# Kernel optimization log

Measured on AMD Instinct MI355X. Metric: run time of the kernel, lower is better.

Reference implementation:

```python
import jax, jax.numpy as jnp
from jax import lax
import numpy as np

INPUT_SIZE, HIDDEN, NUM_LAYERS, NUM_CLASSES = 128, 256, 2, 100
B, T = 256, 512


def _lstm_layer(x, W_ih, W_hh, b_ih, b_hh):
    # x: [B, T, in]; W_ih: [4H, in]; W_hh: [4H, H]; gate order i,f,g,o (PyTorch)
    Bsz = x.shape[0]
    H = W_hh.shape[1]
    x_proj = jnp.einsum('bti,gi->btg', x, W_ih) + b_ih + b_hh  # [B, T, 4H]
    h0 = jnp.zeros((Bsz, H), x.dtype)
    c0 = jnp.zeros((Bsz, H), x.dtype)

    def step(carry, xt):
        h, c = carry
        gates = xt + h @ W_hh.T  # [B, 4H]
        i, f, g, o = jnp.split(gates, 4, axis=-1)
        i = jax.nn.sigmoid(i)
        f = jax.nn.sigmoid(f)
        g = jnp.tanh(g)
        o = jax.nn.sigmoid(o)
        c = f * c + i * g
        h = o * jnp.tanh(c)
        return (h, c), h

    _, hs = lax.scan(step, (h0, c0), jnp.swapaxes(x_proj, 0, 1))  # hs: [T, B, H]
    return jnp.swapaxes(hs, 0, 1)  # [B, T, H]


def setup_inputs() -> dict:
    key = jax.random.key(0)
    ks = jax.random.split(key, 12)
    s_in = 1.0 / np.sqrt(HIDDEN)
    inp = {
        'x': jax.random.normal(ks[0], (B, T, INPUT_SIZE), jnp.float32),
        'W_ih0': jax.random.uniform(ks[1], (4 * HIDDEN, INPUT_SIZE), jnp.float32, -s_in, s_in),
        'W_hh0': jax.random.uniform(ks[2], (4 * HIDDEN, HIDDEN), jnp.float32, -s_in, s_in),
        'b_ih0': jax.random.uniform(ks[3], (4 * HIDDEN,), jnp.float32, -s_in, s_in),
        'b_hh0': jax.random.uniform(ks[4], (4 * HIDDEN,), jnp.float32, -s_in, s_in),
        'W_ih1': jax.random.uniform(ks[5], (4 * HIDDEN, HIDDEN), jnp.float32, -s_in, s_in),
        'W_hh1': jax.random.uniform(ks[6], (4 * HIDDEN, HIDDEN), jnp.float32, -s_in, s_in),
        'b_ih1': jax.random.uniform(ks[7], (4 * HIDDEN,), jnp.float32, -s_in, s_in),
        'b_hh1': jax.random.uniform(ks[8], (4 * HIDDEN,), jnp.float32, -s_in, s_in),
        'fc_w': jax.random.uniform(ks[9], (NUM_CLASSES, HIDDEN), jnp.float32, -s_in, s_in),
        'fc_b': jax.random.uniform(ks[10], (NUM_CLASSES,), jnp.float32, -s_in, s_in),
    }
    return inp


def reference(x, W_ih0, W_hh0, b_ih0, b_hh0, W_ih1, W_hh1, b_ih1, b_hh1, fc_w, fc_b):
    h = _lstm_layer(x, W_ih0, W_hh0, b_ih0, b_hh0)
    h = _lstm_layer(h, W_ih1, W_hh1, b_ih1, b_hh1)
    return h[:, -1, :] @ fc_w.T + fc_b  # [B, num_classes]
```

## Files before the change

### kernel.cpp

```cpp
#include <hip/hip_runtime.h>
#include <math.h>

namespace {

constexpr int kB  = 256;
constexpr int kT  = 512;
constexpr int kIn = 128;
constexpr int kH  = 256;
constexpr int kG  = 1024;
constexpr int kNC = 100;
constexpr int kCT = 64;
constexpr int kNCh = kT / kCT;

typedef __bf16 bf16x8 __attribute__((ext_vector_type(8)));
typedef float f32x4 __attribute__((ext_vector_type(4)));
typedef int i32x4 __attribute__((ext_vector_type(4)));
typedef unsigned short u16;
static_assert(sizeof(bf16x8) == 16, "bf16x8 must be 4 VGPRs");

__device__ __forceinline__ float sigm(float x) {
  return __builtin_amdgcn_rcpf(1.0f + __expf(-x));
}
__device__ __forceinline__ float tanh_f(float x) {
  const float e = __expf(-2.0f * x);
  return (1.0f - e) * __builtin_amdgcn_rcpf(1.0f + e);
}
__device__ __forceinline__ u16 f2bf(float f) {
  return __builtin_bit_cast(u16, (__bf16)f);
}
__device__ __forceinline__ float bf2f(u16 v) {
  return __builtin_bit_cast(float, ((unsigned)v) << 16);
}

__device__ __forceinline__ void glds16(const void* g, void* l) {
  __builtin_amdgcn_global_load_lds(
      (const __attribute__((address_space(1))) void*)g,
      (__attribute__((address_space(3))) void*)l, 16, 0, 0);
}
__device__ __forceinline__ void glds16_llc(const void* g, void* l) {
  __builtin_amdgcn_global_load_lds(
      (const __attribute__((address_space(1))) void*)g,
      (__attribute__((address_space(3))) void*)l, 16, 0, 17);
}
__device__ __forceinline__ void st_bf16_llc(u16* p, u16 v) {
  asm volatile("global_store_short %0, %1, off sc0 sc1"
               :: "v"((unsigned long long)(uintptr_t)p), "v"(v) : "memory");
}
__device__ __forceinline__ void st_i32_llc(int* p, int v) {
  asm volatile("global_store_dword %0, %1, off sc0 sc1"
               :: "v"((unsigned long long)(uintptr_t)p), "v"(v) : "memory");
}
__device__ __forceinline__ int poll16_min(const int* p) {
  i32x4 a, b, c, d;
  asm volatile(
      "global_load_dwordx4 %0, %4, off sc0 sc1\n\t"
      "global_load_dwordx4 %1, %5, off sc0 sc1\n\t"
      "global_load_dwordx4 %2, %6, off sc0 sc1\n\t"
      "global_load_dwordx4 %3, %7, off sc0 sc1\n\t"
      "s_waitcnt vmcnt(0)"
      : "=v"(a), "=v"(b), "=v"(c), "=v"(d)
      : "v"((unsigned long long)(uintptr_t)p),
        "v"((unsigned long long)(uintptr_t)(p + 4)),
        "v"((unsigned long long)(uintptr_t)(p + 8)),
        "v"((unsigned long long)(uintptr_t)(p + 12))
      : "memory");
  int m = a.x;
  m = min(m, a.y); m = min(m, a.z); m = min(m, a.w);
  m = min(m, b.x); m = min(m, b.y); m = min(m, b.z); m = min(m, b.w);
  m = min(m, c.x); m = min(m, c.y); m = min(m, c.z); m = min(m, c.w);
  m = min(m, d.x); m = min(m, d.y); m = min(m, d.z); m = min(m, d.w);
  return m;
}

__global__ __launch_bounds__(256) void pack_whh_frag(
    const float* __restrict__ whh, u16* __restrict__ wpk) {
  const int idx = blockIdx.x * 256 + threadIdx.x;
  const int e  = idx & 7;
  const int l  = (idx >> 3) & 63;
  const int kb = (idx >> 9) & 7;
  const int g  = (idx >> 12) & 3;
  const int wv = idx >> 14;
  const int n = (g << 8) | (wv << 4) | (l & 15);
  const int k = (kb << 5) | (((l >> 4) & 3) << 3) | e;
  wpk[idx] = f2bf(whh[n * kH + k]);
}

template <int K>
__global__ __launch_bounds__(256) void pack_wih_frag(
    const float* __restrict__ w, u16* __restrict__ wp) {
  constexpr int kbBits = (K == 128) ? 2 : 3;
  const int idx = blockIdx.x * 256 + threadIdx.x;
  const int e  = idx & 7;
  const int l  = (idx >> 3) & 63;
  const int kb = (idx >> 9) & ((K / 32) - 1);
  const int n16 = idx >> (9 + kbBits);
  const int n = (n16 << 4) | (l & 15);
  const int k = (kb << 5) | (((l >> 4) & 3) << 3) | e;
  wp[idx] = f2bf(w[n * K + k]);
}

__global__ __launch_bounds__(256) void conv_x(
    const float* __restrict__ x, u16* __restrict__ xbf) {
  const int f4 = blockIdx.x * 256 + threadIdx.x;
  const int rowid = f4 >> 5;
  const int c4 = f4 & 31;
  const int b = rowid >> 9, t = rowid & 511;
  const float4 v = reinterpret_cast<const float4*>(x)[f4];
  ushort4 o;
  o.x = f2bf(v.x); o.y = f2bf(v.y); o.z = f2bf(v.z); o.w = f2bf(v.w);
  reinterpret_cast<ushort4*>(xbf)[(t * 256 + b) * 32 + c4] = o;
}

template <int K>
__global__ __launch_bounds__(256, 4) void gemm_mfma(
    const u16* __restrict__ A, const u16* __restrict__ Bp,
    const float* __restrict__ b1, const float* __restrict__ b2,
    u16* __restrict__ P2) {
  constexpr int NKB = K / 32;
  const int g = blockIdx.x, mt = blockIdx.y;
  const int tt = mt >> 2, bq = mt & 3;
  const int tid = threadIdx.x, w = tid >> 6, l = tid & 63;

  __shared__ __align__(16) unsigned char smem[40960];
  u16* albuf = (u16*)smem;
  u16* bbuf  = (u16*)(smem + 8192);
  u16* sout  = (u16*)smem;

  const u16* Ab = A + ((size_t)(tt * 256 + bq * 64 + w * 16 + (l & 15))) * K +
                  ((l >> 4) & 3) * 8;
  const u16* Bb = Bp + ((size_t)((g * 16 + w * 4) * NKB) * 64 + l) * 8;

  float bb[4];
#pragma unroll
  for (int j = 0; j < 4; ++j) {
    const int n = g * 256 + (w * 4 + j) * 16 + (l & 15);
    bb[j] = b1[n] + b2[n];
  }

  f32x4 acc[4][4];
#pragma unroll
  for (int mf = 0; mf < 4; ++mf)
#pragma unroll
    for (int nf = 0; nf < 4; ++nf) acc[mf][nf] = f32x4{0.f, 0.f, 0.f, 0.f};

#define STAGE(kb, buf)                                                     \
  {                                                                        \
    glds16(Ab + (kb) * 32, albuf + ((buf) * 4 + w) * 512);                 \
    _Pragma("unroll") for (int j = 0; j < 4; ++j)                          \
        glds16(Bb + ((size_t)(j * NKB + (kb)) * 64) * 8,                   \
               bbuf + ((buf) * 16 + w * 4 + j) * 512);                     \
  }

  STAGE(0, 0);
#pragma unroll
  for (int kb = 0; kb < NKB; ++kb) {
    __syncthreads();
    if (kb + 1 < NKB) STAGE(kb + 1, (kb + 1) & 1);
    const int buf = kb & 1;
    bf16x8 af[4], bf[4];
#pragma unroll
    for (int mf = 0; mf < 4; ++mf)
      af[mf] = *reinterpret_cast<const bf16x8*>(albuf + (buf * 4 + mf) * 512 + l * 8);
#pragma unroll
    for (int nf = 0; nf < 4; ++nf)
      bf[nf] = *reinterpret_cast<const bf16x8*>(bbuf + (buf * 16 + w * 4 + nf) * 512 + l * 8);
#pragma unroll
    for (int mf = 0; mf < 4; ++mf)
#pragma unroll
      for (int nf = 0; nf < 4; ++nf)
        acc[mf][nf] = __builtin_amdgcn_mfma_f32_16x16x32_bf16(
            af[mf], bf[nf], acc[mf][nf], 0, 0, 0);
  }
#undef STAGE

  __syncthreads();
#pragma unroll
  for (int mf = 0; mf < 4; ++mf)
#pragma unroll
    for (int nf = 0; nf < 4; ++nf) {
      ushort4 p;
      p.x = f2bf(acc[mf][nf][0] + bb[nf]);
      p.y = f2bf(acc[mf][nf][1] + bb[nf]);
      p.z = f2bf(acc[mf][nf][2] + bb[nf]);
      p.w = f2bf(acc[mf][nf][3] + bb[nf]);
      *reinterpret_cast<ushort4*>(
          sout + (mf * 16 + w * 4 + nf) * 256 + (l & 15) * 16 + ((l >> 4) & 3) * 4) = p;
    }
  __syncthreads();
#pragma unroll
  for (int i = 0; i < 8; ++i) {
    const int chunk = i * 8 + (tid >> 5);
    const int mf = chunk >> 4, wc = chunk & 15;
    const size_t dst =
        ((((size_t)(bq * 4 + mf) * 64 + tt) * 16 + wc) * 4 + g) * 256 +
        (tid & 31) * 8;
    *reinterpret_cast<uint4*>(P2 + dst) =
        *reinterpret_cast<const uint4*>(sout + (mf * 16 + wc) * 256 + (tid & 31) * 8);
  }
}

__global__ __launch_bounds__(256, 1) void lstm_rec_dual(
    const u16* __restrict__ P2_0, const u16* __restrict__ wpk_0,
    float* __restrict__ cs_0, u16* __restrict__ Ho_0, float* __restrict__ hl_0,
    u16* __restrict__ hx_0, int* __restrict__ tg_0, int first_0,
    const u16* __restrict__ P2_1, const u16* __restrict__ wpk_1,
    float* __restrict__ cs_1, u16* __restrict__ Ho_1, float* __restrict__ hl_1,
    u16* __restrict__ hx_1, int* __restrict__ tg_1, int first_1) {
  const int role = blockIdx.x >> 6;
  const u16* P2  = role ? P2_1 : P2_0;
  if (!P2) return;
  const u16* wpk = role ? wpk_1 : wpk_0;
  float* cstate  = role ? cs_1 : cs_0;
  u16* HoutBf    = role ? Ho_1 : Ho_0;
  float* hlast   = role ? hl_1 : hl_0;
  u16* hx        = role ? hx_1 : hx_0;
  int* tags      = role ? tg_1 : tg_0;
  const int first = role ? first_1 : first_0;

  const int bid6 = blockIdx.x & 63;
  const int tid = threadIdx.x;
  const int ug = tid >> 6;
  const int l  = tid & 63;
  const int bblk = bid6 & 15;
  const int hs   = bid6 >> 4;
  const int R0 = bblk << 4;
  const int wv16 = (hs << 2) | ug;
  const int jj = (wv16 << 4) | (l & 15);
  const int mg = ((l >> 4) & 3) << 2;
  const int rowb = R0 + mg;

  __shared__ __align__(16) u16 albuf[2][8][512];

  int* tgb = tags + bblk * 1024;
  u16* hx0 = hx;
  u16* hx1 = hx + (size_t)kB * kH;

  bf16x8 wr[4][8];
#pragma unroll
  for (int g = 0; g < 4; ++g)
#pragma unroll
    for (int kb = 0; kb < 8; ++kb) {
      wr[g][kb] = *reinterpret_cast<const bf16x8*>(
          wpk + (size_t)(((wv16 * 4 + g) * 8 + kb) * 64 + l) * 8);
      asm volatile("" : "+v"(wr[g][kb]));
    }

  f32x4 c4;
  float hnew[4];
  if (first) {
#pragma unroll
    for (int r = 0; r < 4; ++r) c4[r] = 0.f;
  } else {
#pragma unroll
    for (int r = 0; r < 4; ++r) c4[r] = cstate[(rowb + r) * kH + jj];
  }

  const u16* __restrict__ Pb =
      P2 + ((size_t)bblk * 64 * 16 + wv16) * 1024 + ((l & 15) << 4) + mg;
  ushort4 pf[4];
#pragma unroll
  for (int g = 0; g < 4; ++g)
    pf[g] = *reinterpret_cast<const ushort4*>(Pb + (g << 8));

  const int gkb = ug << 1;
#define ISSUE_GLDS(buf, bsel)                                               \
  {                                                                         \
    _Pragma("unroll") for (int q = 0; q < 2; ++q) {                         \
      const int kb = gkb + q;                                               \
      glds16_llc((buf) + ((size_t)(R0 + (l & 15))) * 256 + kb * 32 +        \
                     ((l >> 4) & 3) * 8,                                    \
                 &albuf[bsel][kb][0]);                                      \
    }                                                                       \
  }

  ISSUE_GLDS(hx0, 0);

  for (int tt = 0; tt < kCT; ++tt) {
    __syncthreads();

    f32x4 acc[4];
#pragma unroll
    for (int g = 0; g < 4; ++g) {
      acc[g][0] = bf2f(pf[g].x);
      acc[g][1] = bf2f(pf[g].y);
      acc[g][2] = bf2f(pf[g].z);
      acc[g][3] = bf2f(pf[g].w);
    }
    if (tt + 1 < kCT) {
#pragma unroll
      for (int g = 0; g < 4; ++g)
        pf[g] = *reinterpret_cast<const ushort4*>(
            Pb + (size_t)(tt + 1) * 16384 + (g << 8));
    }

    const u16* ab = &albuf[tt & 1][0][0];
#pragma unroll
    for (int kb = 0; kb < 8; ++kb) {
      const bf16x8 a = *reinterpret_cast<const bf16x8*>(ab + kb * 512 + l * 8);
      acc[0] = __builtin_amdgcn_mfma_f32_16x16x32_bf16(a, wr[0][kb], acc[0], 0, 0, 0);
      acc[1] = __builtin_amdgcn_mfma_f32_16x16x32_bf16(a, wr[1][kb], acc[1], 0, 0, 0);
      acc[2] = __builtin_amdgcn_mfma_f32_16x16x32_bf16(a, wr[2][kb], acc[2], 0, 0, 0);
      acc[3] = __builtin_amdgcn_mfma_f32_16x16x32_bf16(a, wr[3][kb], acc[3], 0, 0, 0);
    }

#pragma unroll
    for (int r = 0; r < 4; ++r) {
      const float ig = sigm(acc[0][r]);
      const float fg = sigm(acc[1][r]);
      const float gg = tanh_f(acc[2][r]);
      const float og = sigm(acc[3][r]);
      const float cc = fg * c4[r] + ig * gg;
      c4[r] = cc;
      hnew[r] = og * tanh_f(cc);
    }

    u16* hw = ((tt + 1) & 1) ? hx1 : hx0;
#pragma unroll
    for (int r = 0; r < 4; ++r)
      st_bf16_llc(hw + ((size_t)(rowb + r) << 8) + jj, f2bf(hnew[r]));

    if (tt + 1 < kCT) {
      const int want = tt + 1;
      asm volatile("s_waitcnt vmcnt(0)" ::: "memory");
      if (l == 0) st_i32_llc(tgb + want * 16 + (hs * 4 + ug), want);
      if (HoutBf) {
#pragma unroll
        for (int r = 0; r < 4; ++r)
          HoutBf[((size_t)tt * 256 + rowb + r) * 256 + jj] = f2bf(hnew[r]);
      }
      while (poll16_min(tgb + want * 16) < want)
        __builtin_amdgcn_s_sleep(1);
      const u16* hr = ((tt + 1) & 1) ? hx1 : hx0;
      ISSUE_GLDS(hr, (tt + 1) & 1);
    } else {
      if (HoutBf) {
#pragma unroll
        for (int r = 0; r < 4; ++r)
          HoutBf[((size_t)tt * 256 + rowb + r) * 256 + jj] = f2bf(hnew[r]);
      }
      if (hlast) {
#pragma unroll
        for (int r = 0; r < 4; ++r)
          hlast[(rowb + r) * kH + jj] = hnew[r];
      }
    }
  }
#undef ISSUE_GLDS

#pragma unroll
  for (int r = 0; r < 4; ++r) cstate[(rowb + r) * kH + jj] = c4[r];
}

__global__ __launch_bounds__(128) void fc_kernel(
    const float* __restrict__ hlast, const float* __restrict__ fcw,
    const float* __restrict__ fcb, float* __restrict__ out) {
  const int b = blockIdx.x;
  const int n = threadIdx.x;
  __shared__ float sh[kH];
  sh[n] = hlast[b * kH + n];
  sh[n + 128] = hlast[b * kH + n + 128];
  __syncthreads();
  if (n < kNC) {
    float a = fcb[n];
    const float* wrow = fcw + n * kH;
#pragma unroll 8
    for (int k = 0; k < kH; ++k) a += sh[k] * wrow[k];
    out[b * kNC + n] = a;
  }
}

}

extern "C" void kernel_launch(void* const* d_in, const int* in_sizes, int n_in,
                              void* d_out, int out_size, void* d_ws, size_t ws_size,
                              hipStream_t stream) {
  (void)in_sizes; (void)n_in; (void)out_size; (void)ws_size;
  const float* x    = (const float*)d_in[0];
  const float* Wih0 = (const float*)d_in[1];
  const float* Whh0 = (const float*)d_in[2];
  const float* bih0 = (const float*)d_in[3];
  const float* bhh0 = (const float*)d_in[4];
  const float* Wih1 = (const float*)d_in[5];
  const float* Whh1 = (const float*)d_in[6];
  const float* bih1 = (const float*)d_in[7];
  const float* bhh1 = (const float*)d_in[8];
  const float* fcw  = (const float*)d_in[9];
  const float* fcb  = (const float*)d_in[10];
  float* out = (float*)d_out;

  char* base = (char*)d_ws;
  size_t off = 0;
  auto take = [&](size_t sz) { char* p = base + off; off += (sz + 255) & ~(size_t)255; return p; };
  const size_t szP2   = (size_t)kB * kCT * kG * 2;
  const size_t szXbf  = (size_t)kT * kB * kIn * 2;
  const size_t szH0   = (size_t)kCT * kB * kH * 2;
  const size_t szC    = (size_t)kB * kH * 4;
  const size_t szHx   = (size_t)2 * kB * kH * 2;
  const size_t szWih0 = (size_t)64 * (kIn / 32) * 512 * 2;
  const size_t szWih1 = (size_t)64 * (kH / 32) * 512 * 2;
  const size_t szWhh  = (size_t)262144 * 2;
  const size_t szTags = (size_t)16 * 16 * 1024 * 4;

  u16* P2a  = (u16*)take(szP2);
  u16* P2b  = (u16*)take(szP2);
  u16* xbf  = (u16*)take(szXbf);
  u16* H0bf = (u16*)take(szH0);
  float* c0s = (float*)take(szC);
  float* c1s = (float*)take(szC);
  float* h1s = (float*)take(szC);
  u16* hxA = (u16*)take(szHx);
  u16* hxB = (u16*)take(szHx);
  u16* WpIh0 = (u16*)take(szWih0);
  u16* WpIh1 = (u16*)take(szWih1);
  u16* Wpk0 = (u16*)take(szWhh);
  u16* Wpk1 = (u16*)take(szWhh);
  int* tags = (int*)take(szTags);

  hipMemsetAsync(tags, 0, szTags, stream);
  hipMemsetAsync(hxA, 0, szHx, stream);
  hipMemsetAsync(hxB, 0, szHx, stream);

  conv_x<<<dim3(16384), dim3(256), 0, stream>>>(x, xbf);
  pack_wih_frag<kIn><<<dim3(512), dim3(256), 0, stream>>>(Wih0, WpIh0);
  pack_wih_frag<kH><<<dim3(1024), dim3(256), 0, stream>>>(Wih1, WpIh1);
  pack_whh_frag<<<dim3(1024), dim3(256), 0, stream>>>(Whh0, Wpk0);
  pack_whh_frag<<<dim3(1024), dim3(256), 0, stream>>>(Whh1, Wpk1);

  auto tslot = [&](int s) { return tags + (size_t)s * 16 * 1024; };

  gemm_mfma<kIn><<<dim3(4, 256), dim3(256), 0, stream>>>(
      xbf, WpIh0, bih0, bhh0, P2a);
  lstm_rec_dual<<<dim3(128), dim3(256), 0, stream>>>(
      P2a, Wpk0, c0s, H0bf, nullptr, hxA, tslot(0), 1,
      nullptr, nullptr, nullptr, nullptr, nullptr, nullptr, nullptr, 0);
  for (int ch = 1; ch < kNCh; ++ch) {
    gemm_mfma<kH><<<dim3(4, 256), dim3(256), 0, stream>>>(
        H0bf, WpIh1, bih1, bhh1, P2b);
    gemm_mfma<kIn><<<dim3(4, 256), dim3(256), 0, stream>>>(
        xbf + (size_t)ch * kCT * kB * kIn, WpIh0, bih0, bhh0, P2a);
    lstm_rec_dual<<<dim3(128), dim3(256), 0, stream>>>(
        P2a, Wpk0, c0s, H0bf, nullptr, hxA, tslot(2 * ch), (ch == 0) ? 1 : 0,
        P2b, Wpk1, c1s, nullptr, h1s, hxB, tslot(2 * (ch - 1) + 1),
        (ch == 1) ? 1 : 0);
  }
  gemm_mfma<kH><<<dim3(4, 256), dim3(256), 0, stream>>>(
      H0bf, WpIh1, bih1, bhh1, P2b);
  lstm_rec_dual<<<dim3(128), dim3(256), 0, stream>>>(
      nullptr, nullptr, nullptr, nullptr, nullptr, nullptr, nullptr, 0,
      P2b, Wpk1, c1s, nullptr, h1s, hxB, tslot(2 * (kNCh - 1) + 1), 0);
  fc_kernel<<<dim3(kB), dim3(128), 0, stream>>>(h1s, fcw, fcb, out);
}
```

Measured before the change: 1.859 ms.

## Process two batch blocks per workgroup in the recurrent LSTM kernel

Halves the recurrent kernel grid by having each workgroup handle two 16-row batch blocks (A and B) in sequence within each timestep. The recurrent weights stay in registers and are reused across both blocks, with separate barrier tags, LDS buffers and cell states per block. The intent is to hide one block's cross-workgroup synchronization latency behind the other block's compute and to use fewer CUs. The cost is that per-timestep work per workgroup doubles on the serial critical path.

Measured after the change: 3.534 ms. 1.9x slower.

```diff
diff --git a/kernel.cpp b/kernel.cpp
--- a/kernel.cpp
+++ b/kernel.cpp
@@ -199,14 +199,14 @@
   }
 }
 
-__global__ __launch_bounds__(256, 1) void lstm_rec_dual(
+__global__ __launch_bounds__(256, 1) void lstm_rec_dual2(
     const u16* __restrict__ P2_0, const u16* __restrict__ wpk_0,
     float* __restrict__ cs_0, u16* __restrict__ Ho_0, float* __restrict__ hl_0,
     u16* __restrict__ hx_0, int* __restrict__ tg_0, int first_0,
     const u16* __restrict__ P2_1, const u16* __restrict__ wpk_1,
     float* __restrict__ cs_1, u16* __restrict__ Ho_1, float* __restrict__ hl_1,
     u16* __restrict__ hx_1, int* __restrict__ tg_1, int first_1) {
-  const int role = blockIdx.x >> 6;
+  const int role = blockIdx.x >> 5;
   const u16* P2  = role ? P2_1 : P2_0;
   if (!P2) return;
   const u16* wpk = role ? wpk_1 : wpk_0;
@@ -217,21 +217,23 @@
   int* tags      = role ? tg_1 : tg_0;
   const int first = role ? first_1 : first_0;
 
-  const int bid6 = blockIdx.x & 63;
+  const int bid5 = blockIdx.x & 31;
   const int tid = threadIdx.x;
   const int ug = tid >> 6;
   const int l  = tid & 63;
-  const int bblk = bid6 & 15;
-  const int hs   = bid6 >> 4;
-  const int R0 = bblk << 4;
+  const int pr = bid5 & 7;
+  const int hs = bid5 >> 3;
+  const int bbA = pr * 2, bbB = pr * 2 + 1;
+  const int R0A = bbA << 4, R0B = bbB << 4;
   const int wv16 = (hs << 2) | ug;
   const int jj = (wv16 << 4) | (l & 15);
   const int mg = ((l >> 4) & 3) << 2;
-  const int rowb = R0 + mg;
-
-  __shared__ __align__(16) u16 albuf[2][8][512];
-
-  int* tgb = tags + bblk * 1024;
+  const int rwA = R0A + mg, rwB = R0B + mg;
+
+  __shared__ __align__(16) u16 albuf[2][2][8][512];
+
+  int* tgA = tags + bbA * 1024;
+  int* tgB = tags + bbB * 1024;
   u16* hx0 = hx;
   u16* hx1 = hx + (size_t)kB * kH;
 
@@ -245,110 +247,163 @@
       asm volatile("" : "+v"(wr[g][kb]));
     }
 
-  f32x4 c4;
+  f32x4 cA, cB;
   float hnew[4];
   if (first) {
 #pragma unroll
-    for (int r = 0; r < 4; ++r) c4[r] = 0.f;
+    for (int r = 0; r < 4; ++r) { cA[r] = 0.f; cB[r] = 0.f; }
   } else {
 #pragma unroll
-    for (int r = 0; r < 4; ++r) c4[r] = cstate[(rowb + r) * kH + jj];
-  }
-
-  const u16* __restrict__ Pb =
-      P2 + ((size_t)bblk * 64 * 16 + wv16) * 1024 + ((l & 15) << 4) + mg;
-  ushort4 pf[4];
-#pragma unroll
-  for (int g = 0; g < 4; ++g)
-    pf[g] = *reinterpret_cast<const ushort4*>(Pb + (g << 8));
+    for (int r = 0; r < 4; ++r) {
+      cA[r] = cstate[(rwA + r) * kH + jj];
+      cB[r] = cstate[(rwB + r) * kH + jj];
+    }
+  }
+
+  const u16* __restrict__ PbA =
+      P2 + ((size_t)bbA * 64 * 16 + wv16) * 1024 + ((l & 15) << 4) + mg;
+  const u16* __restrict__ PbB =
+      P2 + ((size_t)bbB * 64 * 16 + wv16) * 1024 + ((l & 15) << 4) + mg;
+  ushort4 pfA[4], pfB[4];
+#pragma unroll
+  for (int g = 0; g < 4; ++g) {
+    pfA[g] = *reinterpret_cast<const ushort4*>(PbA + (g << 8));
+    pfB[g] = *reinterpret_cast<const ushort4*>(PbB + (g << 8));
+  }
 
   const int gkb = ug << 1;
-#define ISSUE_GLDS(buf, bsel)                                               \
+#define ISSUE_GLDS(bg, R0, buf, bsel)                                       \
   {                                                                         \
     _Pragma("unroll") for (int q = 0; q < 2; ++q) {                         \
       const int kb = gkb + q;                                               \
-      glds16_llc((buf) + ((size_t)(R0 + (l & 15))) * 256 + kb * 32 +        \
+      glds16_llc((buf) + ((size_t)((R0) + (l & 15))) * 256 + kb * 32 +      \
                      ((l >> 4) & 3) * 8,                                    \
-                 &albuf[bsel][kb][0]);                                      \
+                 &albuf[bg][bsel][kb][0]);                                  \
     }                                                                       \
   }
 
-  ISSUE_GLDS(hx0, 0);
+  ISSUE_GLDS(0, R0A, hx0, 0);
+  ISSUE_GLDS(1, R0B, hx0, 0);
 
   for (int tt = 0; tt < kCT; ++tt) {
     __syncthreads();
-
-    f32x4 acc[4];
-#pragma unroll
-    for (int g = 0; g < 4; ++g) {
-      acc[g][0] = bf2f(pf[g].x);
-      acc[g][1] = bf2f(pf[g].y);
-      acc[g][2] = bf2f(pf[g].z);
-      acc[g][3] = bf2f(pf[g].w);
+    const int nxt = tt + 1;
+    const bool more = (nxt < kCT);
+    u16* hw = (nxt & 1) ? hx1 : hx0;
+
+    {
+      f32x4 acc[4];
+#pragma unroll
+      for (int g = 0; g < 4; ++g) {
+        acc[g][0] = bf2f(pfA[g].x); acc[g][1] = bf2f(pfA[g].y);
+        acc[g][2] = bf2f(pfA[g].z); acc[g][3] = bf2f(pfA[g].w);
+      }
+      if (more) {
+#pragma unroll
+        for (int g = 0; g < 4; ++g)
+          pfA[g] = *reinterpret_cast<const ushort4*>(
+              PbA + (size_t)nxt * 16384 + (g << 8));
+      }
+      const u16* ab = &albuf[0][tt & 1][0][0];
+#pragma unroll
+      for (int kb = 0; kb < 8; ++kb) {
+        const bf16x8 a = *reinterpret_cast<const bf16x8*>(ab + kb * 512 + l * 8);
+        acc[0] = __builtin_amdgcn_mfma_f32_16x16x32_bf16(a, wr[0][kb], acc[0], 0, 0, 0);
+        acc[1] = __builtin_amdgcn_mfma_f32_16x16x32_bf16(a, wr[1][kb], acc[1], 0, 0, 0);
+        acc[2] = __builtin_amdgcn_mfma_f32_16x16x32_bf16(a, wr[2][kb], acc[2], 0, 0, 0);
+        acc[3] = __builtin_amdgcn_mfma_f32_16x16x32_bf16(a, wr[3][kb], acc[3], 0, 0, 0);
+      }
+#pragma unroll
+      for (int r = 0; r < 4; ++r) {
+        const float ig = sigm(acc[0][r]);
+        const float fg = sigm(acc[1][r]);
+        const float gg = tanh_f(acc[2][r]);
+        const float og = sigm(acc[3][r]);
+        const float cc = fg * cA[r] + ig * gg;
+        cA[r] = cc;
+        hnew[r] = og * tanh_f(cc);
+      }
+#pragma unroll
+      for (int r = 0; r < 4; ++r)
+        st_bf16_llc(hw + ((size_t)(rwA + r) << 8) + jj, f2bf(hnew[r]));
+      if (more) {
+        asm volatile("s_waitcnt vmcnt(0)" ::: "memory");
+        if (l == 0) st_i32_llc(tgA + nxt * 16 + wv16, nxt);
+        while (poll16_min(tgA + nxt * 16) < nxt)
+          __builtin_amdgcn_s_sleep(1);
+        ISSUE_GLDS(0, R0A, hw, nxt & 1);
+      }
+      if (HoutBf) {
+#pragma unroll
+        for (int r = 0; r < 4; ++r)
+          HoutBf[((size_t)tt * 256 + rwA + r) * 256 + jj] = f2bf(hnew[r]);
+      }
+      if (!more && hlast) {
+#pragma unroll
+        for (int r = 0; r < 4; ++r) hlast[(rwA + r) * kH + jj] = hnew[r];
+      }
     }
-    if (tt + 1 < kCT) {
-#pragma unroll
-      for (int g = 0; g < 4; ++g)
-        pf[g] = *reinterpret_cast<const ushort4*>(
-            Pb + (size_t)(tt + 1) * 16384 + (g << 8));
+
+    {
+      f32x4 acc[4];
+#pragma unroll
+      for (int g = 0; g < 4; ++g) {
+        acc[g][0] = bf2f(pfB[g].x); acc[g][1] = bf2f(pfB[g].y);
+        acc[g][2] = bf2f(pfB[g].z); acc[g][3] = bf2f(pfB[g].w);
+      }
+      if (more) {
+#pragma unroll
+        for (int g = 0; g < 4; ++g)
+          pfB[g] = *reinterpret_cast<const ushort4*>(
+              PbB + (size_t)nxt * 16384 + (g << 8));
+      }
+      const u16* ab = &albuf[1][tt & 1][0][0];
+#pragma unroll
+      for (int kb = 0; kb < 8; ++kb) {
+        const bf16x8 a = *reinterpret_cast<const bf16x8*>(ab + kb * 512 + l * 8);
+        acc[0] = __builtin_amdgcn_mfma_f32_16x16x32_bf16(a, wr[0][kb], acc[0], 0, 0, 0);
+        acc[1] = __builtin_amdgcn_mfma_f32_16x16x32_bf16(a, wr[1][kb], acc[1], 0, 0, 0);
+        acc[2] = __builtin_amdgcn_mfma_f32_16x16x32_bf16(a, wr[2][kb], acc[2], 0, 0, 0);
+        acc[3] = __builtin_amdgcn_mfma_f32_16x16x32_bf16(a, wr[3][kb], acc[3], 0, 0, 0);
+      }
+#pragma unroll
+      for (int r = 0; r < 4; ++r) {
+        const float ig = sigm(acc[0][r]);
+        const float fg = sigm(acc[1][r]);
+        const float gg = tanh_f(acc[2][r]);
+        const float og = sigm(acc[3][r]);
+        const float cc = fg * cB[r] + ig * gg;
+        cB[r] = cc;
+        hnew[r] = og * tanh_f(cc);
+      }
+#pragma unroll
+      for (int r = 0; r < 4; ++r)
+        st_bf16_llc(hw + ((size_t)(rwB + r) << 8) + jj, f2bf(hnew[r]));
+      if (more) {
+        asm volatile("s_waitcnt vmcnt(0)" ::: "memory");
+        if (l == 0) st_i32_llc(tgB + nxt * 16 + wv16, nxt);
+        while (poll16_min(tgB + nxt * 16) < nxt)
+          __builtin_amdgcn_s_sleep(1);
+        ISSUE_GLDS(1, R0B, hw, nxt & 1);
+      }
+      if (HoutBf) {
+#pragma unroll
+        for (int r = 0; r < 4; ++r)
+          HoutBf[((size_t)tt * 256 + rwB + r) * 256 + jj] = f2bf(hnew[r]);
+      }
+      if (!more && hlast) {
+#pragma unroll
+        for (int r = 0; r < 4; ++r) hlast[(rwB + r) * kH + jj] = hnew[r];
+      }
     }
-
-    const u16* ab = &albuf[tt & 1][0][0];
-#pragma unroll
-    for (int kb = 0; kb < 8; ++kb) {
-      const bf16x8 a = *reinterpret_cast<const bf16x8*>(ab + kb * 512 + l * 8);
-      acc[0] = __builtin_amdgcn_mfma_f32_16x16x32_bf16(a, wr[0][kb], acc[0], 0, 0, 0);
-      acc[1] = __builtin_amdgcn_mfma_f32_16x16x32_bf16(a, wr[1][kb], acc[1], 0, 0, 0);
-      acc[2] = __builtin_amdgcn_mfma_f32_16x16x32_bf16(a, wr[2][kb], acc[2], 0, 0, 0);
-      acc[3] = __builtin_amdgcn_mfma_f32_16x16x32_bf16(a, wr[3][kb], acc[3], 0, 0, 0);
-    }
-
-#pragma unroll
-    for (int r = 0; r < 4; ++r) {
-      const float ig = sigm(acc[0][r]);
-      const float fg = sigm(acc[1][r]);
-      const float gg = tanh_f(acc[2][r]);
-      const float og = sigm(acc[3][r]);
-      const float cc = fg * c4[r] + ig * gg;
-      c4[r] = cc;
-      hnew[r] = og * tanh_f(cc);
-    }
-
-    u16* hw = ((tt + 1) & 1) ? hx1 : hx0;
-#pragma unroll
-    for (int r = 0; r < 4; ++r)
-      st_bf16_llc(hw + ((size_t)(rowb + r) << 8) + jj, f2bf(hnew[r]));
-
-    if (tt + 1 < kCT) {
-      const int want = tt + 1;
-      asm volatile("s_waitcnt vmcnt(0)" ::: "memory");
-      if (l == 0) st_i32_llc(tgb + want * 16 + (hs * 4 + ug), want);
-      if (HoutBf) {
-#pragma unroll
-        for (int r = 0; r < 4; ++r)
-          HoutBf[((size_t)tt * 256 + rowb + r) * 256 + jj] = f2bf(hnew[r]);
-      }
-      while (poll16_min(tgb + want * 16) < want)
-        __builtin_amdgcn_s_sleep(1);
-      const u16* hr = ((tt + 1) & 1) ? hx1 : hx0;
-      ISSUE_GLDS(hr, (tt + 1) & 1);
-    } else {
-      if (HoutBf) {
-#pragma unroll
-        for (int r = 0; r < 4; ++r)
-          HoutBf[((size_t)tt * 256 + rowb + r) * 256 + jj] = f2bf(hnew[r]);
-      }
-      if (hlast) {
-#pragma unroll
-        for (int r = 0; r < 4; ++r)
-          hlast[(rowb + r) * kH + jj] = hnew[r];
-      }
-    }
   }
 #undef ISSUE_GLDS
 
 #pragma unroll
-  for (int r = 0; r < 4; ++r) cstate[(rowb + r) * kH + jj] = c4[r];
+  for (int r = 0; r < 4; ++r) {
+    cstate[(rwA + r) * kH + jj] = cA[r];
+    cstate[(rwB + r) * kH + jj] = cB[r];
+  }
 }
 
 __global__ __launch_bounds__(128) void fc_kernel(
@@ -430,7 +485,7 @@
 
   gemm_mfma<kIn><<<dim3(4, 256), dim3(256), 0, stream>>>(
       xbf, WpIh0, bih0, bhh0, P2a);
-  lstm_rec_dual<<<dim3(128), dim3(256), 0, stream>>>(
+  lstm_rec_dual2<<<dim3(64), dim3(256), 0, stream>>>(
       P2a, Wpk0, c0s, H0bf, nullptr, hxA, tslot(0), 1,
       nullptr, nullptr, nullptr, nullptr, nullptr, nullptr, nullptr, 0);
   for (int ch = 1; ch < kNCh; ++ch) {
@@ -438,14 +493,14 @@
         H0bf, WpIh1, bih1, bhh1, P2b);
     gemm_mfma<kIn><<<dim3(4, 256), dim3(256), 0, stream>>>(
         xbf + (size_t)ch * kCT * kB * kIn, WpIh0, bih0, bhh0, P2a);
-    lstm_rec_dual<<<dim3(128), dim3(256), 0, stream>>>(
-        P2a, Wpk0, c0s, H0bf, nullptr, hxA, tslot(2 * ch), (ch == 0) ? 1 : 0,
+    lstm_rec_dual2<<<dim3(64), dim3(256), 0, stream>>>(
+        P2a, Wpk0, c0s, H0bf, nullptr, hxA, tslot(2 * ch), 0,
         P2b, Wpk1, c1s, nullptr, h1s, hxB, tslot(2 * (ch - 1) + 1),
         (ch == 1) ? 1 : 0);
   }
   gemm_mfma<kH><<<dim3(4, 256), dim3(256), 0, stream>>>(
       H0bf, WpIh1, bih1, bhh1, P2b);
-  lstm_rec_dual<<<dim3(128), dim3(256), 0, stream>>>(
+  lstm_rec_dual2<<<dim3(64), dim3(256), 0, stream>>>(
       nullptr, nullptr, nullptr, nullptr, nullptr, nullptr, nullptr, 0,
       P2b, Wpk1, c1s, nullptr, h1s, hxB, tslot(2 * (kNCh - 1) + 1), 0);
   fc_kernel<<<dim3(kB), dim3(128), 0, stream>>>(h1s, fcw, fcb, out);
```

## Replace tag-counter barrier with sentinel-poll on a four-slot h ring buffer

Applied to the files above, without the earlier changes.

The recurrent kernel no longer publishes per-step tag counters, spins on a 16-entry minimum, then stages the next hidden state through LDS with a workgroup barrier. Each wave now polls the bf16 hidden-state slice it needs directly from a four-slot ring in global memory. A slot counts as ready once none of its values equals the +inf bf16 sentinel, and the loaded registers feed the MFMA without going through LDS. Each wave also re-arms the slot two steps ahead with sentinels. This removes a store-then-poll round trip and the __syncthreads per timestep. The costs are wider polling loads, a spin guard that gives up silently after a fixed count, and correctness that relies on h never equalling the sentinel.

New measurement: 2.778 ms. 1.49x slower.

```diff
diff --git a/kernel.cpp b/kernel.cpp
--- a/kernel.cpp
+++ b/kernel.cpp
@@ -11,6 +11,7 @@
 constexpr int kNC = 100;
 constexpr int kCT = 64;
 constexpr int kNCh = kT / kCT;
+constexpr unsigned kSent = 0x7F80u;
 
 typedef __bf16 bf16x8 __attribute__((ext_vector_type(8)));
 typedef float f32x4 __attribute__((ext_vector_type(4)));
@@ -37,39 +38,35 @@
       (const __attribute__((address_space(1))) void*)g,
       (__attribute__((address_space(3))) void*)l, 16, 0, 0);
 }
-__device__ __forceinline__ void glds16_llc(const void* g, void* l) {
-  __builtin_amdgcn_global_load_lds(
-      (const __attribute__((address_space(1))) void*)g,
-      (__attribute__((address_space(3))) void*)l, 16, 0, 17);
-}
 __device__ __forceinline__ void st_bf16_llc(u16* p, u16 v) {
   asm volatile("global_store_short %0, %1, off sc0 sc1"
                :: "v"((unsigned long long)(uintptr_t)p), "v"(v) : "memory");
 }
-__device__ __forceinline__ void st_i32_llc(int* p, int v) {
-  asm volatile("global_store_dword %0, %1, off sc0 sc1"
-               :: "v"((unsigned long long)(uintptr_t)p), "v"(v) : "memory");
-}
-__device__ __forceinline__ int poll16_min(const int* p) {
-  i32x4 a, b, c, d;
+__device__ __forceinline__ void poll_load8(const u16* p, i32x4 v[8]) {
   asm volatile(
-      "global_load_dwordx4 %0, %4, off sc0 sc1\n\t"
-      "global_load_dwordx4 %1, %5, off sc0 sc1\n\t"
-      "global_load_dwordx4 %2, %6, off sc0 sc1\n\t"
-      "global_load_dwordx4 %3, %7, off sc0 sc1\n\t"
+      "global_load_dwordx4 %0, %8, off sc0 sc1\n\t"
+      "global_load_dwordx4 %1, %8, off offset:64 sc0 sc1\n\t"
+      "global_load_dwordx4 %2, %8, off offset:128 sc0 sc1\n\t"
+      "global_load_dwordx4 %3, %8, off offset:192 sc0 sc1\n\t"
+      "global_load_dwordx4 %4, %8, off offset:256 sc0 sc1\n\t"
+      "global_load_dwordx4 %5, %8, off offset:320 sc0 sc1\n\t"
+      "global_load_dwordx4 %6, %8, off offset:384 sc0 sc1\n\t"
+      "global_load_dwordx4 %7, %8, off offset:448 sc0 sc1\n\t"
       "s_waitcnt vmcnt(0)"
-      : "=v"(a), "=v"(b), "=v"(c), "=v"(d)
-      : "v"((unsigned long long)(uintptr_t)p),
-        "v"((unsigned long long)(uintptr_t)(p + 4)),
-        "v"((unsigned long long)(uintptr_t)(p + 8)),
-        "v"((unsigned long long)(uintptr_t)(p + 12))
+      : "=v"(v[0]), "=v"(v[1]), "=v"(v[2]), "=v"(v[3]),
+        "=v"(v[4]), "=v"(v[5]), "=v"(v[6]), "=v"(v[7])
+      : "v"((unsigned long long)(uintptr_t)p)
       : "memory");
-  int m = a.x;
-  m = min(m, a.y); m = min(m, a.z); m = min(m, a.w);
-  m = min(m, b.x); m = min(m, b.y); m = min(m, b.z); m = min(m, b.w);
-  m = min(m, c.x); m = min(m, c.y); m = min(m, c.z); m = min(m, c.w);
-  m = min(m, d.x); m = min(m, d.y); m = min(m, d.z); m = min(m, d.w);
-  return m;
+}
+__device__ __forceinline__ bool chunk_ok(const i32x4 v) {
+  bool ok = true;
+#pragma unroll
+  for (int i = 0; i < 4; ++i) {
+    const unsigned u = (unsigned)v[i];
+    ok = ok && ((u & 0xFFFFu) != kSent);
+    ok = ok && ((u >> 16) != kSent);
+  }
+  return ok;
 }
 
 __global__ __launch_bounds__(256) void pack_whh_frag(
@@ -111,6 +108,11 @@
   reinterpret_cast<ushort4*>(xbf)[(t * 256 + b) * 32 + c4] = o;
 }
 
+__global__ __launch_bounds__(256) void init_hx(u16* __restrict__ hx) {
+  const int i = blockIdx.x * 256 + threadIdx.x;
+  hx[i] = (i < 65536) ? (u16)0 : (u16)kSent;
+}
+
 template <int K>
 __global__ __launch_bounds__(256, 4) void gemm_mfma(
     const u16* __restrict__ A, const u16* __restrict__ Bp,
@@ -199,13 +201,13 @@
   }
 }
 
-__global__ __launch_bounds__(256, 1) void lstm_rec_dual(
+__global__ __launch_bounds__(256, 1) void lstm_rec_poll(
     const u16* __restrict__ P2_0, const u16* __restrict__ wpk_0,
     float* __restrict__ cs_0, u16* __restrict__ Ho_0, float* __restrict__ hl_0,
-    u16* __restrict__ hx_0, int* __restrict__ tg_0, int first_0,
+    u16* __restrict__ hx_0, int first_0,
     const u16* __restrict__ P2_1, const u16* __restrict__ wpk_1,
     float* __restrict__ cs_1, u16* __restrict__ Ho_1, float* __restrict__ hl_1,
-    u16* __restrict__ hx_1, int* __restrict__ tg_1, int first_1) {
+    u16* __restrict__ hx_1, int first_1) {
   const int role = blockIdx.x >> 6;
   const u16* P2  = role ? P2_1 : P2_0;
   if (!P2) return;
@@ -214,7 +216,6 @@
   u16* HoutBf    = role ? Ho_1 : Ho_0;
   float* hlast   = role ? hl_1 : hl_0;
   u16* hx        = role ? hx_1 : hx_0;
-  int* tags      = role ? tg_1 : tg_0;
   const int first = role ? first_1 : first_0;
 
   const int bid6 = blockIdx.x & 63;
@@ -228,12 +229,7 @@
   const int jj = (wv16 << 4) | (l & 15);
   const int mg = ((l >> 4) & 3) << 2;
   const int rowb = R0 + mg;
-
-  __shared__ __align__(16) u16 albuf[2][8][512];
-
-  int* tgb = tags + bblk * 1024;
-  u16* hx0 = hx;
-  u16* hx1 = hx + (size_t)kB * kH;
+  const int poff = (R0 + (l & 15)) * 256 + ((l >> 4) & 3) * 8;
 
   bf16x8 wr[4][8];
 #pragma unroll
@@ -262,21 +258,26 @@
   for (int g = 0; g < 4; ++g)
     pf[g] = *reinterpret_cast<const ushort4*>(Pb + (g << 8));
 
-  const int gkb = ug << 1;
-#define ISSUE_GLDS(buf, bsel)                                               \
-  {                                                                         \
-    _Pragma("unroll") for (int q = 0; q < 2; ++q) {                         \
-      const int kb = gkb + q;                                               \
-      glds16_llc((buf) + ((size_t)(R0 + (l & 15))) * 256 + kb * 32 +        \
-                     ((l >> 4) & 3) * 8,                                    \
-                 &albuf[bsel][kb][0]);                                      \
-    }                                                                       \
-  }
-
-  ISSUE_GLDS(hx0, 0);
-
   for (int tt = 0; tt < kCT; ++tt) {
-    __syncthreads();
+    i32x4 av[8];
+    {
+      const u16* pb = hx + ((tt & 3) << 16) + poff;
+      int guard = 0;
+      for (;;) {
+        poll_load8(pb, av);
+        bool ok = true;
+#pragma unroll
+        for (int kb = 0; kb < 8; ++kb) ok = ok && chunk_ok(av[kb]);
+        if (ok || ++guard > (1 << 16)) break;
+      }
+    }
+
+    {
+      u16* rf = hx + (((tt + 2) & 3) << 16);
+#pragma unroll
+      for (int r = 0; r < 4; ++r)
+        st_bf16_llc(rf + ((size_t)(rowb + r) << 8) + jj, (u16)kSent);
+    }
 
     f32x4 acc[4];
 #pragma unroll
@@ -286,23 +287,22 @@
       acc[g][2] = bf2f(pf[g].z);
       acc[g][3] = bf2f(pf[g].w);
     }
-    if (tt + 1 < kCT) {
+    const bool more = (tt + 1 < kCT);
+    if (more) {
 #pragma unroll
       for (int g = 0; g < 4; ++g)
         pf[g] = *reinterpret_cast<const ushort4*>(
             Pb + (size_t)(tt + 1) * 16384 + (g << 8));
     }
 
-    const u16* ab = &albuf[tt & 1][0][0];
 #pragma unroll
     for (int kb = 0; kb < 8; ++kb) {
-      const bf16x8 a = *reinterpret_cast<const bf16x8*>(ab + kb * 512 + l * 8);
+      const bf16x8 a = __builtin_bit_cast(bf16x8, av[kb]);
       acc[0] = __builtin_amdgcn_mfma_f32_16x16x32_bf16(a, wr[0][kb], acc[0], 0, 0, 0);
       acc[1] = __builtin_amdgcn_mfma_f32_16x16x32_bf16(a, wr[1][kb], acc[1], 0, 0, 0);
       acc[2] = __builtin_amdgcn_mfma_f32_16x16x32_bf16(a, wr[2][kb], acc[2], 0, 0, 0);
       acc[3] = __builtin_amdgcn_mfma_f32_16x16x32_bf16(a, wr[3][kb], acc[3], 0, 0, 0);
     }
-
 #pragma unroll
     for (int r = 0; r < 4; ++r) {
       const float ig = sigm(acc[0][r]);
@@ -314,38 +314,27 @@
       hnew[r] = og * tanh_f(cc);
     }
 
-    u16* hw = ((tt + 1) & 1) ? hx1 : hx0;
-#pragma unroll
-    for (int r = 0; r < 4; ++r)
-      st_bf16_llc(hw + ((size_t)(rowb + r) << 8) + jj, f2bf(hnew[r]));
-
-    if (tt + 1 < kCT) {
-      const int want = tt + 1;
-      asm volatile("s_waitcnt vmcnt(0)" ::: "memory");
-      if (l == 0) st_i32_llc(tgb + want * 16 + (hs * 4 + ug), want);
-      if (HoutBf) {
-#pragma unroll
-        for (int r = 0; r < 4; ++r)
-          HoutBf[((size_t)tt * 256 + rowb + r) * 256 + jj] = f2bf(hnew[r]);
-      }
-      while (poll16_min(tgb + want * 16) < want)
-        __builtin_amdgcn_s_sleep(1);
-      const u16* hr = ((tt + 1) & 1) ? hx1 : hx0;
-      ISSUE_GLDS(hr, (tt + 1) & 1);
-    } else {
-      if (HoutBf) {
-#pragma unroll
-        for (int r = 0; r < 4; ++r)
-          HoutBf[((size_t)tt * 256 + rowb + r) * 256 + jj] = f2bf(hnew[r]);
-      }
-      if (hlast) {
-#pragma unroll
-        for (int r = 0; r < 4; ++r)
-          hlast[(rowb + r) * kH + jj] = hnew[r];
-      }
-    }
-  }
-#undef ISSUE_GLDS
+    if (more) asm volatile("s_waitcnt vmcnt(4)" ::: "memory");
+    else      asm volatile("s_waitcnt vmcnt(0)" ::: "memory");
+
+    {
+      u16* hw = hx + (((tt + 1) & 3) << 16);
+#pragma unroll
+      for (int r = 0; r < 4; ++r)
+        st_bf16_llc(hw + ((size_t)(rowb + r) << 8) + jj, f2bf(hnew[r]));
+    }
+
+    if (HoutBf) {
+#pragma unroll
+      for (int r = 0; r < 4; ++r)
+        HoutBf[((size_t)tt * 256 + rowb + r) * 256 + jj] = f2bf(hnew[r]);
+    }
+    if (!more && hlast) {
+#pragma unroll
+      for (int r = 0; r < 4; ++r)
+        hlast[(rowb + r) * kH + jj] = hnew[r];
+    }
+  }
 
 #pragma unroll
   for (int r = 0; r < 4; ++r) cstate[(rowb + r) * kH + jj] = c4[r];
@@ -395,11 +384,10 @@
   const size_t szXbf  = (size_t)kT * kB * kIn * 2;
   const size_t szH0   = (size_t)kCT * kB * kH * 2;
   const size_t szC    = (size_t)kB * kH * 4;
-  const size_t szHx   = (size_t)2 * kB * kH * 2;
+  const size_t szHx   = (size_t)4 * kB * kH * 2;
   const size_t szWih0 = (size_t)64 * (kIn / 32) * 512 * 2;
   const size_t szWih1 = (size_t)64 * (kH / 32) * 512 * 2;
   const size_t szWhh  = (size_t)262144 * 2;
-  const size_t szTags = (size_t)16 * 16 * 1024 * 4;
 
   u16* P2a  = (u16*)take(szP2);
   u16* P2b  = (u16*)take(szP2);
@@ -414,11 +402,9 @@
   u16* WpIh1 = (u16*)take(szWih1);
   u16* Wpk0 = (u16*)take(szWhh);
   u16* Wpk1 = (u16*)take(szWhh);
-  int* tags = (int*)take(szTags);
-
-  hipMemsetAsync(tags, 0, szTags, stream);
-  hipMemsetAsync(hxA, 0, szHx, stream);
-  hipMemsetAsync(hxB, 0, szHx, stream);
+
+  init_hx<<<dim3(1024), dim3(256), 0, stream>>>(hxA);
+  init_hx<<<dim3(1024), dim3(256), 0, stream>>>(hxB);
 
   conv_x<<<dim3(16384), dim3(256), 0, stream>>>(x, xbf);
   pack_wih_frag<kIn><<<dim3(512), dim3(256), 0, stream>>>(Wih0, WpIh0);
@@ -426,27 +412,24 @@
   pack_whh_frag<<<dim3(1024), dim3(256), 0, stream>>>(Whh0, Wpk0);
   pack_whh_frag<<<dim3(1024), dim3(256), 0, stream>>>(Whh1, Wpk1);
 
-  auto tslot = [&](int s) { return tags + (size_t)s * 16 * 1024; };
-
   gemm_mfma<kIn><<<dim3(4, 256), dim3(256), 0, stream>>>(
       xbf, WpIh0, bih0, bhh0, P2a);
-  lstm_rec_dual<<<dim3(128), dim3(256), 0, stream>>>(
-      P2a, Wpk0, c0s, H0bf, nullptr, hxA, tslot(0), 1,
-      nullptr, nullptr, nullptr, nullptr, nullptr, nullptr, nullptr, 0);
+  lstm_rec_poll<<<dim3(128), dim3(256), 0, stream>>>(
+      P2a, Wpk0, c0s, H0bf, nullptr, hxA, 1,
+      nullptr, nullptr, nullptr, nullptr, nullptr, nullptr, 0);
   for (int ch = 1; ch < kNCh; ++ch) {
     gemm_mfma<kH><<<dim3(4, 256), dim3(256), 0, stream>>>(
         H0bf, WpIh1, bih1, bhh1, P2b);
     gemm_mfma<kIn><<<dim3(4, 256), dim3(256), 0, stream>>>(
         xbf + (size_t)ch * kCT * kB * kIn, WpIh0, bih0, bhh0, P2a);
-    lstm_rec_dual<<<dim3(128), dim3(256), 0, stream>>>(
-        P2a, Wpk0, c0s, H0bf, nullptr, hxA, tslot(2 * ch), (ch == 0) ? 1 : 0,
-        P2b, Wpk1, c1s, nullptr, h1s, hxB, tslot(2 * (ch - 1) + 1),
-        (ch == 1) ? 1 : 0);
+    lstm_rec_poll<<<dim3(128), dim3(256), 0, stream>>>(
+        P2a, Wpk0, c0s, H0bf, nullptr, hxA, 0,
+        P2b, Wpk1, c1s, nullptr, h1s, hxB, (ch == 1) ? 1 : 0);
   }
   gemm_mfma<kH><<<dim3(4, 256), dim3(256), 0, stream>>>(
       H0bf, WpIh1, bih1, bhh1, P2b);
-  lstm_rec_dual<<<dim3(128), dim3(256), 0, stream>>>(
-      nullptr, nullptr, nullptr, nullptr, nullptr, nullptr, nullptr, 0,
-      P2b, Wpk1, c1s, nullptr, h1s, hxB, tslot(2 * (kNCh - 1) + 1), 0);
+  lstm_rec_poll<<<dim3(128), dim3(256), 0, stream>>>(
+      nullptr, nullptr, nullptr, nullptr, nullptr, nullptr, 0,
+      P2b, Wpk1, c1s, nullptr, h1s, hxB, 0);
   fc_kernel<<<dim3(kB), dim3(128), 0, stream>>>(h1s, fcw, fcb, out);
 }
```

## Load recurrent h fragments directly into registers, drop LDS staging and block barrier

Applied to the files above, without the earlier changes.

Each wave now reads its 8 bf16x8 A-fragments of the previous hidden state straight from global memory into VGPRs with coherent (sc0 sc1) loads, instead of staging them through a double-buffered LDS tile filled by global_load_lds. This removes the per-step __syncthreads and the LDS round trip on the serial recurrence path. The polling loop now sleeps only every 256 spins and gives up after about a million spins, which lowers wake-up latency but can let a wave read stale h if the bound is hit. Each wave reloads all fragments itself, so the block issues four times the global traffic per step.

New measurement: 2.465 ms. 32.6% more time.

```diff
diff --git a/kernel.cpp b/kernel.cpp
--- a/kernel.cpp
+++ b/kernel.cpp
@@ -37,11 +37,6 @@
       (const __attribute__((address_space(1))) void*)g,
       (__attribute__((address_space(3))) void*)l, 16, 0, 0);
 }
-__device__ __forceinline__ void glds16_llc(const void* g, void* l) {
-  __builtin_amdgcn_global_load_lds(
-      (const __attribute__((address_space(1))) void*)g,
-      (__attribute__((address_space(3))) void*)l, 16, 0, 17);
-}
 __device__ __forceinline__ void st_bf16_llc(u16* p, u16 v) {
   asm volatile("global_store_short %0, %1, off sc0 sc1"
                :: "v"((unsigned long long)(uintptr_t)p), "v"(v) : "memory");
@@ -49,6 +44,22 @@
 __device__ __forceinline__ void st_i32_llc(int* p, int v) {
   asm volatile("global_store_dword %0, %1, off sc0 sc1"
                :: "v"((unsigned long long)(uintptr_t)p), "v"(v) : "memory");
+}
+__device__ __forceinline__ void load_afrag8(const u16* p, i32x4 v[8]) {
+  asm volatile(
+      "global_load_dwordx4 %0, %8, off sc0 sc1\n\t"
+      "global_load_dwordx4 %1, %8, off offset:64 sc0 sc1\n\t"
+      "global_load_dwordx4 %2, %8, off offset:128 sc0 sc1\n\t"
+      "global_load_dwordx4 %3, %8, off offset:192 sc0 sc1\n\t"
+      "global_load_dwordx4 %4, %8, off offset:256 sc0 sc1\n\t"
+      "global_load_dwordx4 %5, %8, off offset:320 sc0 sc1\n\t"
+      "global_load_dwordx4 %6, %8, off offset:384 sc0 sc1\n\t"
+      "global_load_dwordx4 %7, %8, off offset:448 sc0 sc1\n\t"
+      "s_waitcnt vmcnt(0)"
+      : "=&v"(v[0]), "=&v"(v[1]), "=&v"(v[2]), "=&v"(v[3]),
+        "=&v"(v[4]), "=&v"(v[5]), "=&v"(v[6]), "=&v"(v[7])
+      : "v"((unsigned long long)(uintptr_t)p)
+      : "memory");
 }
 __device__ __forceinline__ int poll16_min(const int* p) {
   i32x4 a, b, c, d;
@@ -58,7 +69,7 @@
       "global_load_dwordx4 %2, %6, off sc0 sc1\n\t"
       "global_load_dwordx4 %3, %7, off sc0 sc1\n\t"
       "s_waitcnt vmcnt(0)"
-      : "=v"(a), "=v"(b), "=v"(c), "=v"(d)
+      : "=&v"(a), "=&v"(b), "=&v"(c), "=&v"(d)
       : "v"((unsigned long long)(uintptr_t)p),
         "v"((unsigned long long)(uintptr_t)(p + 4)),
         "v"((unsigned long long)(uintptr_t)(p + 8)),
@@ -228,8 +239,7 @@
   const int jj = (wv16 << 4) | (l & 15);
   const int mg = ((l >> 4) & 3) << 2;
   const int rowb = R0 + mg;
-
-  __shared__ __align__(16) u16 albuf[2][8][512];
+  const int poff = (R0 + (l & 15)) * 256 + ((l >> 4) & 3) * 8;
 
   int* tgb = tags + bblk * 1024;
   u16* hx0 = hx;
@@ -262,22 +272,10 @@
   for (int g = 0; g < 4; ++g)
     pf[g] = *reinterpret_cast<const ushort4*>(Pb + (g << 8));
 
-  const int gkb = ug << 1;
-#define ISSUE_GLDS(buf, bsel)                                               \
-  {                                                                         \
-    _Pragma("unroll") for (int q = 0; q < 2; ++q) {                         \
-      const int kb = gkb + q;                                               \
-      glds16_llc((buf) + ((size_t)(R0 + (l & 15))) * 256 + kb * 32 +        \
-                     ((l >> 4) & 3) * 8,                                    \
-                 &albuf[bsel][kb][0]);                                      \
-    }                                                                       \
-  }
-
-  ISSUE_GLDS(hx0, 0);
+  i32x4 av[8];
+  load_afrag8(hx0 + poff, av);
 
   for (int tt = 0; tt < kCT; ++tt) {
-    __syncthreads();
-
     f32x4 acc[4];
 #pragma unroll
     for (int g = 0; g < 4; ++g) {
@@ -286,17 +284,17 @@
       acc[g][2] = bf2f(pf[g].z);
       acc[g][3] = bf2f(pf[g].w);
     }
-    if (tt + 1 < kCT) {
+    const bool more = (tt + 1 < kCT);
+    if (more) {
 #pragma unroll
       for (int g = 0; g < 4; ++g)
         pf[g] = *reinterpret_cast<const ushort4*>(
             Pb + (size_t)(tt + 1) * 16384 + (g << 8));
     }
 
-    const u16* ab = &albuf[tt & 1][0][0];
 #pragma unroll
     for (int kb = 0; kb < 8; ++kb) {
-      const bf16x8 a = *reinterpret_cast<const bf16x8*>(ab + kb * 512 + l * 8);
+      const bf16x8 a = __builtin_bit_cast(bf16x8, av[kb]);
       acc[0] = __builtin_amdgcn_mfma_f32_16x16x32_bf16(a, wr[0][kb], acc[0], 0, 0, 0);
       acc[1] = __builtin_amdgcn_mfma_f32_16x16x32_bf16(a, wr[1][kb], acc[1], 0, 0, 0);
       acc[2] = __builtin_amdgcn_mfma_f32_16x16x32_bf16(a, wr[2][kb], acc[2], 0, 0, 0);
@@ -319,19 +317,22 @@
     for (int r = 0; r < 4; ++r)
       st_bf16_llc(hw + ((size_t)(rowb + r) << 8) + jj, f2bf(hnew[r]));
 
-    if (tt + 1 < kCT) {
+    if (more) {
       const int want = tt + 1;
       asm volatile("s_waitcnt vmcnt(0)" ::: "memory");
-      if (l == 0) st_i32_llc(tgb + want * 16 + (hs * 4 + ug), want);
+      if (l == 0) st_i32_llc(tgb + want * 16 + wv16, want);
       if (HoutBf) {
 #pragma unroll
         for (int r = 0; r < 4; ++r)
           HoutBf[((size_t)tt * 256 + rowb + r) * 256 + jj] = f2bf(hnew[r]);
       }
-      while (poll16_min(tgb + want * 16) < want)
-        __builtin_amdgcn_s_sleep(1);
-      const u16* hr = ((tt + 1) & 1) ? hx1 : hx0;
-      ISSUE_GLDS(hr, (tt + 1) & 1);
+      int spin = 0;
+      for (;;) {
+        if (poll16_min(tgb + want * 16) >= want) break;
+        if ((++spin & 255) == 0) __builtin_amdgcn_s_sleep(1);
+        if (spin > (1 << 20)) break;
+      }
+      load_afrag8(hw + poff, av);
     } else {
       if (HoutBf) {
 #pragma unroll
@@ -345,7 +346,6 @@
       }
     }
   }
-#undef ISSUE_GLDS
 
 #pragma unroll
   for (int r = 0; r < 4; ++r) cstate[(rowb + r) * kH + jj] = c4[r];
@@ -439,7 +439,7 @@
     gemm_mfma<kIn><<<dim3(4, 256), dim3(256), 0, stream>>>(
         xbf + (size_t)ch * kCT * kB * kIn, WpIh0, bih0, bhh0, P2a);
     lstm_rec_dual<<<dim3(128), dim3(256), 0, stream>>>(
-        P2a, Wpk0, c0s, H0bf, nullptr, hxA, tslot(2 * ch), (ch == 0) ? 1 : 0,
+        P2a, Wpk0, c0s, H0bf, nullptr, hxA, tslot(2 * ch), 0,
         P2b, Wpk1, c1s, nullptr, h1s, hxB, tslot(2 * (ch - 1) + 1),
         (ch == 1) ? 1 : 0);
   }
```
